# Performance work log

Measured on AMD Instinct MI355X. Metric: run time of the kernel, lower is better.

The kernel has to match this reference:

```python
import jax, jax.numpy as jnp
import numpy as np

B, T, D = 4, 1024, 512
H, TD = 4, 5
DH = D // H          # per-head value dim
DFF = D // 2         # Clifford FFN half-width
DR = D               # reservoir size
M = 64               # 2**mem_depth leaves
OFFSETS = (-3, -2, -1, 0)  # causal sheaf window=3
EPS = 1e-5

def _ln(x, g, b):
    m = jnp.mean(x, axis=-1, keepdims=True)
    v = jnp.mean((x - m) ** 2, axis=-1, keepdims=True)
    return (x - m) / jnp.sqrt(v + EPS) * g + b

def setup_inputs() -> dict:
    keys = iter(jax.random.split(jax.random.key(0), 64))
    def rn(shape, s=0.02):
        return (jax.random.normal(next(keys), shape) * s).astype(jnp.float32)
    x = jax.random.normal(next(keys), (B, T, D), dtype=jnp.float32)
    # sparse reservoir recurrence matrix (sparsity=0.9)
    wres_mask = (jax.random.uniform(next(keys), (DR, DR)) > 0.9).astype(jnp.float32)
    res_Wres = jax.random.normal(next(keys), (DR, DR)) * wres_mask * 0.05
    eye = jnp.eye(D, dtype=jnp.float32)
    sheaf_Rw = jnp.stack([eye + rn((D, D), 0.01) for _ in OFFSETS])  # [4,D,D]
    return dict(
        x=x,
        ln1_g=jnp.ones((D,)), ln1_b=jnp.zeros((D,)),
        ln2_g=jnp.ones((D,)), ln2_b=jnp.zeros((D,)),
        ln3_g=jnp.ones((D,)), ln3_b=jnp.zeros((D,)),
        ln4_g=jnp.ones((D,)), ln4_b=jnp.zeros((D,)),
        attn_Wp=rn((H * TD, D)), attn_bp=jnp.zeros((H * TD,)),
        attn_Wv=rn((D, D)), attn_Wo=rn((D, D)),
        ffn_Wr=rn((DFF, D)), ffn_br=jnp.zeros((DFF,)),
        ffn_Wi=rn((DFF, D)), ffn_bi=jnp.zeros((DFF,)),
        ffn_Wg=rn((D, D)), ffn_bg=jnp.zeros((D,)),
        ffn_Wout=rn((D, D)), ffn_bout=jnp.zeros((D,)),
        res_Win=rn((DR, D)), res_Wres=res_Wres,
        res_logrho=jnp.float32(0.0), res_leak=jnp.float32(0.3),
        res_readout=rn((D, DR)),
        res_v0=jax.random.normal(next(keys), (DR,), dtype=jnp.float32),
        mem_keys=rn((M, D)), mem_vals=rn((M, D)),
        mem_Wq=rn((D, D)), mem_Wout=rn((D, D)), mem_bout=jnp.zeros((D,)),
        sheaf_Rw=sheaf_Rw, sheaf_Rb=jnp.zeros((len(OFFSETS), D)),
        sheaf_alpha=jnp.float32(0.15),
    )

def reference(x, ln1_g, ln1_b, ln2_g, ln2_b, ln3_g, ln3_b, ln4_g, ln4_b,
              attn_Wp, attn_bp, attn_Wv, attn_Wo,
              ffn_Wr, ffn_br, ffn_Wi, ffn_bi, ffn_Wg, ffn_bg, ffn_Wout, ffn_bout,
              res_Win, res_Wres, res_logrho, res_leak, res_readout, res_v0,
              mem_keys, mem_vals, mem_Wq, mem_Wout, mem_bout,
              sheaf_Rw, sheaf_Rb, sheaf_alpha):
    Bx, Tx, d = x.shape

    def attn_fn(h):  # PAdicAttention, causal
        paths = jax.nn.sigmoid(h @ attn_Wp.T + attn_bp)
        paths = paths.reshape(Bx, Tx, H, TD).transpose(0, 2, 1, 3)   # [B,H,T,TD]
        pq = paths[:, :, :, None, :]
        pk = paths[:, :, None, :, :]
        agree = pq * pk + (1.0 - pq) * (1.0 - pk)                    # [B,H,T,T,TD]
        sim = jnp.sum(jnp.cumprod(agree, axis=-1), axis=-1) / TD     # [B,H,T,T]
        mask = jnp.triu(jnp.ones((Tx, Tx), bool), 1)
        sim = jnp.where(mask[None, None], -jnp.inf, sim)
        a = jax.nn.softmax(sim, axis=-1)
        V = (h @ attn_Wv.T).reshape(Bx, Tx, H, DH).transpose(0, 2, 1, 3)
        ctx = jnp.einsum('bhqk,bhkd->bhqd', a, V)
        return ctx.transpose(0, 2, 1, 3).reshape(Bx, Tx, d) @ attn_Wo.T

    def res_fn(h):  # EchoStateReservoir
        rho_t = jax.nn.sigmoid(res_logrho) * 1.5
        Wd = jax.lax.stop_gradient(res_Wres)
        def pi(v, _):
            v = Wd @ v
            n = jnp.linalg.norm(v)
            return jnp.where(n > 0, v / n, v), None
        v, _ = jax.lax.scan(pi, res_v0, None, length=3)
        rho_c = jax.lax.stop_gradient(jnp.linalg.norm(Wd @ v))
        Ws = res_Wres * (rho_t / jnp.maximum(rho_c, 1e-6))
        lk = jax.nn.sigmoid(res_leak)
        u = h @ res_Win.T                                            # [B,T,dr]
        def step(hs, ut):
            hs = (1.0 - lk) * hs + lk * jnp.tanh(hs @ Ws.T + ut)
            return hs, hs
        _, Hs = jax.lax.scan(step, jnp.zeros((Bx, DR), x.dtype), u.transpose(1, 0, 2))
        return Hs.transpose(1, 0, 2) @ res_readout.T

    def mem_fn(h):  # PAdicMemory
        q = h @ mem_Wq.T
        w = jax.nn.softmax(q @ mem_keys.T / jnp.sqrt(jnp.float32(d)), axis=-1)
        return (w @ mem_vals) @ mem_Wout.T + mem_bout

    def ffn_fn(h):  # CliffordFFN
        r = h @ ffn_Wr.T + ffn_br
        i = h @ ffn_Wi.T + ffn_bi
        prod = jnp.concatenate([r * r - i * i, 2.0 * r * i], axis=-1)
        gate = jax.nn.sigmoid(h @ ffn_Wg.T + ffn_bg)
        return (prod * gate) @ ffn_Wout.T + ffn_bout

    def sheaf_fn(h):  # SheafDiffusion, causal offsets
        lap = jnp.zeros_like(h)
        for idx, delta in enumerate(OFFSETS):
            Rx = h @ sheaf_Rw[idx].T + sheaf_Rb[idx]
            if delta == 0:
                x_nb = h
            else:
                ad = -delta
                x_nb = jnp.concatenate(
                    [jnp.zeros((Bx, ad, d), h.dtype), h[:, :Tx - ad, :]], axis=1)
            lap = lap + (Rx - x_nb) @ sheaf_Rw[idx]   # note: @ W, not W.T (as in source)
        return h - jnp.abs(sheaf_alpha) * lap

    x = x + attn_fn(_ln(x, ln1_g, ln1_b))
    x = x + res_fn(_ln(x, ln2_g, ln2_b))
    x = x + mem_fn(_ln(x, ln3_g, ln3_b))
    x = x + ffn_fn(_ln(x, ln4_g, ln4_b))
    return sheaf_fn(x)
```

## Files before the change

kernel.cpp:

```cpp
#include <hip/hip_runtime.h>
#include <hip/hip_bf16.h>
#include <stdint.h>

typedef unsigned short u16;
typedef unsigned int u32;
typedef unsigned long long u64;
typedef __bf16 bf16x8 __attribute__((ext_vector_type(8)));
typedef float f32x4 __attribute__((ext_vector_type(4)));
typedef int i32x4 __attribute__((ext_vector_type(4)));

__device__ __forceinline__ u16 f2bf(float f){
  unsigned u = __float_as_uint(f);
  u += 0x7fffu + ((u>>16)&1u);
  return (u16)(u>>16);
}
__device__ __forceinline__ float bf2f(u16 h){ return __uint_as_float((u32)h<<16); }
__device__ __forceinline__ float sigm(float x){ return 1.f/(1.f+__expf(-x)); }
__device__ __forceinline__ float tanh_fast(float x){ float e = __expf(2.f*x); return 1.f - 2.f/(e+1.f); }

__device__ __forceinline__ void gl_lds16(const void* g, void* l){
  __builtin_amdgcn_global_load_lds((const __attribute__((address_space(1))) void*)g,
                                   (__attribute__((address_space(3))) void*)l, 16, 0, 0);
}


__global__ __launch_bounds__(128) void prep_weights(
  const float* Wp, const float* Wv, const float* Wo, const float* Win, const float* rd,
  const float* Wq, const float* keys, const float* vals, const float* mWo,
  const float* Wr, const float* Wi, const float* Wg, const float* fWo, const float* Rw,
  const float* bp, const float* fbr, const float* fbi, const float* fbg,
  u16* WpB, u16* WvB, u16* WoB, u16* WinB, u16* rdB,
  u16* WqB, u16* keysB, u16* valsB, u16* mWoB,
  u16* WrB, u16* WiB, u16* WgB, u16* fWoB, u16* RwB,
  float* bpp, float* bpc, float* ss)
{
  int blk = blockIdx.x, t = threadIdx.x;
  if(blk==6912){ if(t<128) bpp[t] = (t<20)? bp[t] : 0.f; return; }
  if(blk==6913){
    for(int j=t; j<1024; j+=128)
      bpc[j] = (j<256)? fbr[j] : (j<512)? fbi[j-256] : fbg[j-512];
    return;
  }
  if(blk==6914){ if(t==0) ss[0]=1.f; else if(t<5) ss[t]=0.f; return; }
  const float* src = nullptr; u16* dst = nullptr; int r;
  bool perm = false;
  if(blk<128){ r=blk; dst=WpB+(size_t)r*512; if(r<20) src=Wp+(size_t)r*512; }
  else if(blk<640){ r=blk-128; dst=WvB+(size_t)r*512; src=Wv+(size_t)r*512; }
  else if(blk<1152){ r=blk-640; dst=WoB+(size_t)r*512; src=Wo+(size_t)r*512; }
  else if(blk<1664){ r=blk-1152; dst=WinB+(size_t)r*512; src=Win+(size_t)r*512; }
  else if(blk<2176){ r=blk-1664; dst=rdB+(size_t)r*512; src=rd+(size_t)r*512; perm=true; }
  else if(blk<2688){ r=blk-2176; dst=WqB+(size_t)r*512; src=Wq+(size_t)r*512; }
  else if(blk<2752){ r=blk-2688; dst=keysB+(size_t)r*512; src=keys+(size_t)r*512; }
  else if(blk<2816){ r=blk-2752; dst=valsB+(size_t)r*512; src=vals+(size_t)r*512; }
  else if(blk<3328){ r=blk-2816; dst=mWoB+(size_t)r*512; src=mWo+(size_t)r*512; }
  else if(blk<3584){ r=blk-3328; dst=WrB+(size_t)r*512; src=Wr+(size_t)r*512; }
  else if(blk<3840){ r=blk-3584; dst=WiB+(size_t)r*512; src=Wi+(size_t)r*512; }
  else if(blk<4352){ r=blk-3840; dst=WgB+(size_t)r*512; src=Wg+(size_t)r*512; }
  else if(blk<4864){ r=blk-4352; dst=fWoB+(size_t)r*512; src=fWo+(size_t)r*512; }
  else { r=blk-4864; dst=RwB+(size_t)r*512; src=Rw+(size_t)r*512; }
  if(src){
    float4 a = *(const float4*)&src[t*4];
    ushort4 o; o.x=f2bf(a.x); o.y=f2bf(a.y); o.z=f2bf(a.z); o.w=f2bf(a.w);
    if(perm){
      int k0 = t*4;
      int base = (k0 & ~63) | ((k0&15)<<2) | ((k0>>4)&3);
      dst[base] = o.x; dst[base+4] = o.y; dst[base+8] = o.z; dst[base+12] = o.w;
    } else {
      *(ushort4*)&dst[t*4] = o;
    }
  } else {
    ushort4 z; z.x=0; z.y=0; z.z=0; z.w=0;
    *(ushort4*)&dst[t*4] = z;
  }
}

__global__ __launch_bounds__(256) void transpose_rw(const float* __restrict__ Rw, u16* __restrict__ RwT){
  __shared__ float tl[32][33];
  int z = blockIdx.z, it = blockIdx.x, jt = blockIdx.y;
  const float* src = Rw + (size_t)z*262144;
  int r = threadIdx.x>>3, c4 = (threadIdx.x&7)*4;
  float4 v = *(const float4*)&src[(size_t)(jt*32+r)*512 + it*32 + c4];
  tl[r][c4+0]=v.x; tl[r][c4+1]=v.y; tl[r][c4+2]=v.z; tl[r][c4+3]=v.w;
  __syncthreads();
  ushort4 o;
  o.x = f2bf(tl[c4+0][r]); o.y = f2bf(tl[c4+1][r]);
  o.z = f2bf(tl[c4+2][r]); o.w = f2bf(tl[c4+3][r]);
  *(ushort4*)&RwT[(size_t)(it*32+r)*2048 + z*512 + jt*32 + c4] = o;
}

__global__ __launch_bounds__(64) void ln_kernel(const float* __restrict__ x, const float* __restrict__ g,
      const float* __restrict__ b, u16* __restrict__ out)
{
  int row = blockIdx.x, lane = threadIdx.x;
  const float* xr = x + (size_t)row*512;
  float4 v0 = *(const float4*)&xr[lane*4];
  float4 v1 = *(const float4*)&xr[256+lane*4];
  float s = v0.x+v0.y+v0.z+v0.w + v1.x+v1.y+v1.z+v1.w;
  float q = v0.x*v0.x+v0.y*v0.y+v0.z*v0.z+v0.w*v0.w + v1.x*v1.x+v1.y*v1.y+v1.z*v1.z+v1.w*v1.w;
  #pragma unroll
  for(int m=1;m<64;m<<=1){ s += __shfl_xor(s,m); q += __shfl_xor(q,m); }
  float mean = s*(1.f/512.f);
  float var  = q*(1.f/512.f) - mean*mean;
  float rstd = rsqrtf(var + 1e-5f);
  float4 g0 = *(const float4*)&g[lane*4], g1 = *(const float4*)&g[256+lane*4];
  float4 b0 = *(const float4*)&b[lane*4], b1 = *(const float4*)&b[256+lane*4];
  ushort4 o0, o1;
  o0.x = f2bf((v0.x-mean)*rstd*g0.x + b0.x); o0.y = f2bf((v0.y-mean)*rstd*g0.y + b0.y);
  o0.z = f2bf((v0.z-mean)*rstd*g0.z + b0.z); o0.w = f2bf((v0.w-mean)*rstd*g0.w + b0.w);
  o1.x = f2bf((v1.x-mean)*rstd*g1.x + b1.x); o1.y = f2bf((v1.y-mean)*rstd*g1.y + b1.y);
  o1.z = f2bf((v1.z-mean)*rstd*g1.z + b1.z); o1.w = f2bf((v1.w-mean)*rstd*g1.w + b1.w);
  *(ushort4*)&out[(size_t)row*512 + lane*4] = o0;
  *(ushort4*)&out[(size_t)row*512 + 256 + lane*4] = o1;
}

template<int EPI>
__global__ __launch_bounds__(256,2) void gemm_nt(
  const u16* __restrict__ A, const u16* __restrict__ Bw, int K, int ldc,
  float* __restrict__ outf, u16* __restrict__ outb,
  const float* __restrict__ bias, const float* __restrict__ resid,
  const float* __restrict__ aux, float* __restrict__ outf2,
  const float* __restrict__ scal, int shift_ad)
{
  __shared__ u16 Al[128*64];
  __shared__ u16 Bl[64*64];
  const int t = threadIdx.x;
  const int bm = blockIdx.x, bn = blockIdx.y;
  const int wid = t>>6, lane = t&63;
  const int wr = wid>>1, wc = wid&1;
  const int fr = lane&15, fq = lane>>4;
  f32x4 acc[4][2] = {};
  const int nK = K>>6;
  const u16* Ab = A + (size_t)(bm*128)*K;
  const u16* Bb = Bw + (size_t)(bn*64)*K;
  const int srow8 = t>>3;
  const int scol = (t&7)*8;
  char* AlB = (char*)Al; char* BlB = (char*)Bl;
  const int lbase = wid*1024;
  for(int bk=0; bk<nK; ++bk){
    #pragma unroll
    for(int c=0;c<4;++c)
      gl_lds16(&Ab[(size_t)(c*32+srow8)*K + bk*64 + scol], AlB + c*4096 + lbase);
    #pragma unroll
    for(int c=0;c<2;++c)
      gl_lds16(&Bb[(size_t)(c*32+srow8)*K + bk*64 + scol], BlB + c*4096 + lbase);
    __syncthreads();
    #pragma unroll
    for(int kk=0;kk<2;++kk){
      bf16x8 af[4], bf[2];
      #pragma unroll
      for(int m=0;m<4;++m) af[m] = *(const bf16x8*)&Al[(wr*64+m*16+fr)*64 + kk*32 + fq*8];
      #pragma unroll
      for(int n=0;n<2;++n) bf[n] = *(const bf16x8*)&Bl[(wc*32+n*16+fr)*64 + kk*32 + fq*8];
      #pragma unroll
      for(int m=0;m<4;++m)
        #pragma unroll
        for(int n=0;n<2;++n)
          acc[m][n] = __builtin_amdgcn_mfma_f32_16x16x32_bf16(af[m], bf[n], acc[m][n], 0,0,0);
    }
    __syncthreads();
  }
  float alpha = 0.f;
  if(EPI==8) alpha = fabsf(scal[0]);
  #pragma unroll
  for(int m=0;m<4;++m){
    int gr0 = bm*128 + wr*64 + m*16 + fq*4;
    #pragma unroll
    for(int n=0;n<2;++n){
      int gc = bn*64 + wc*32 + n*16 + fr;
      float bv = 0.f;
      if(EPI==2||EPI==3||EPI==5||EPI==6||EPI==9||EPI==12) bv = bias[gc];
      if(EPI==10 && gc<128) bv = bias[gc];
      #pragma unroll
      for(int i=0;i<4;++i){
        int r = gr0 + i;
        float v = acc[m][n][i] + bv;
        if(EPI==3) v = sigm(v);
        if(EPI==1||EPI==5||EPI==6) v += resid[(size_t)r*ldc + gc];
        if(EPI==8){
          outf[(size_t)r*ldc + gc] -= alpha*v;
        } else if(EPI==9){
          if(gc<512) outf[(size_t)r*512 + gc] = v;
          else       outf2[(size_t)r*512 + gc-512] = sigm(v);
        } else if(EPI==10){
          if(gc<128) outf[(size_t)r*128 + gc] = sigm(v);
          else       outf2[(size_t)r*512 + gc-128] = v;
        } else if(EPI==11){
          int pc = (gc & ~63) | ((gc&15)<<2) | ((gc>>4)&3);
          outf[(size_t)r*512 + pc] = v;
        } else if(EPI==12){
          int idx = gc>>9;
          int ad = 3 - idx;
          int ts = r & 1023;
          float xnb = 0.f;
          if(ts >= ad) xnb = bf2f(((const u16*)aux)[(size_t)(r-ad)*512 + (gc&511)]);
          outb[(size_t)r*2048 + gc] = f2bf(v - xnb);
        } else {
          if(EPI==0||EPI==1||EPI==2||EPI==3||EPI==5) outf[(size_t)r*ldc + gc] = v;
          if(EPI==6) outf2[(size_t)r*ldc + gc] = v;
          if(EPI==4||EPI==6) outb[(size_t)r*ldc + gc] = f2bf(v);
        }
      }
    }
  }
}

__global__ __launch_bounds__(128) void attn_kernel(
  const float* __restrict__ paths, const float* __restrict__ Vbuf, u16* __restrict__ ctxb)
{
  const int t = threadIdx.x;
  const int qt = blockIdx.x, bh = blockIdx.y;
  const int b = bh>>2, h = bh&3;
  const int rb = b<<10;
  const int ql = t>>2, sub = t&3;
  const int q = qt*32 + ql;
  const int wid = t>>6, lane = t&63;
  const int fr = lane&15, fq = lane>>4;
  __shared__ u16 Vl[128][72];
  __shared__ u16 Pl[32][72];
  __shared__ float pkl[64][6];
  __shared__ float scl[32];
  __shared__ float lsm[32];
  float al[5], bl[5];
  #pragma unroll
  for(int l=0;l<5;++l){
    float p = paths[(size_t)(rb+q)*128 + h*5 + l];
    al[l] = 2.f*p - 1.f; bl[l] = 1.f - p;
  }
  float m_run = -1e30f, l_run = 0.f;
  f32x4 acc[2][4] = {};
  const int nkt = (qt>>1) + 1;
  for(int kt=0; kt<nkt; ++kt){
    int k0 = kt*64;
    for(int i=t; i<320; i+=128){
      int k = i/5, l = i%5;
      pkl[k][l] = paths[(size_t)(rb+k0+k)*128 + h*5 + l];
    }
    {
      int dg = (t&31)*4, kbase = t>>5;
      #pragma unroll
      for(int i=0;i<16;++i){
        int k = kbase + i*4;
        float4 v4 = *(const float4*)&Vbuf[(size_t)(rb+k0+k)*512 + h*128 + dg];
        Vl[dg+0][k] = f2bf(v4.x); Vl[dg+1][k] = f2bf(v4.y);
        Vl[dg+2][k] = f2bf(v4.z); Vl[dg+3][k] = f2bf(v4.w);
      }
    }
    __syncthreads();
    float pj[16]; float tm = -1e30f;
    #pragma unroll
    for(int j=0;j<16;++j){
      int kidx = sub*16 + j;
      int k = k0 + kidx;
      float s;
      if(k <= q){
        float c = al[0]*pkl[kidx][0] + bl[0];
        float sa = c;
        #pragma unroll
        for(int l=1;l<5;++l){ c *= al[l]*pkl[kidx][l] + bl[l]; sa += c; }
        s = sa*0.2f;
      } else s = -1e30f;
      pj[j] = s; tm = fmaxf(tm, s);
    }
    tm = fmaxf(tm, __shfl_xor(tm,1,4));
    tm = fmaxf(tm, __shfl_xor(tm,2,4));
    float m_new = fmaxf(m_run, tm);
    float corr = __expf(m_run - m_new);
    float ls = 0.f;
    #pragma unroll
    for(int j=0;j<16;++j){
      float p = (pj[j] > -1e29f) ? __expf(pj[j]-m_new) : 0.f;
      ls += p;
      Pl[ql][sub*16+j] = f2bf(p);
    }
    l_run = l_run*corr + ls;
    m_run = m_new;
    if(sub==0) scl[ql] = corr;
    __syncthreads();
    #pragma unroll
    for(int m=0;m<2;++m){
      float c0 = scl[m*16+fq*4+0], c1 = scl[m*16+fq*4+1];
      float c2 = scl[m*16+fq*4+2], c3 = scl[m*16+fq*4+3];
      #pragma unroll
      for(int n=0;n<4;++n){ acc[m][n][0]*=c0; acc[m][n][1]*=c1; acc[m][n][2]*=c2; acc[m][n][3]*=c3; }
    }
    #pragma unroll
    for(int kk=0;kk<2;++kk){
      bf16x8 af[2], bf[4];
      #pragma unroll
      for(int m=0;m<2;++m) af[m] = *(const bf16x8*)&Pl[m*16+fr][kk*32+fq*8];
      #pragma unroll
      for(int n=0;n<4;++n) bf[n] = *(const bf16x8*)&Vl[wid*64+n*16+fr][kk*32+fq*8];
      #pragma unroll
      for(int m=0;m<2;++m)
        #pragma unroll
        for(int n=0;n<4;++n)
          acc[m][n] = __builtin_amdgcn_mfma_f32_16x16x32_bf16(af[m], bf[n], acc[m][n], 0,0,0);
    }
    __syncthreads();
  }
  {
    float lt = l_run + __shfl_xor(l_run,1,4);
    lt += __shfl_xor(lt,2,4);
    if(sub==0) lsm[ql] = lt;
  }
  __syncthreads();
  #pragma unroll
  for(int m=0;m<2;++m){
    float inv[4];
    #pragma unroll
    for(int i=0;i<4;++i) inv[i] = 1.f/lsm[m*16+fq*4+i];
    #pragma unroll
    for(int n=0;n<4;++n){
      int row = rb + qt*32 + m*16 + fq*4;
      int col = h*128 + wid*64 + n*16 + fr;
      #pragma unroll
      for(int i=0;i<4;++i)
        ctxb[(size_t)(row+i)*512 + col] = f2bf(acc[m][n][i]*inv[i]);
    }
  }
}

__global__ __launch_bounds__(256) void pmv(const float* __restrict__ W, const float* __restrict__ vin,
                    const float* __restrict__ ssin, float* __restrict__ vout, float* __restrict__ ssout)
{
  __shared__ float vs[512];
  int t = threadIdx.x;
  int j = blockIdx.x*16 + (t>>4), ks = t&15;
  float s = ssin[0];
  float inv = (s>0.f)? rsqrtf(s) : 1.f;
  vs[t] = vin[t]*inv; vs[t+256] = vin[t+256]*inv;
  __syncthreads();
  float p = 0.f;
  const float* wr = &W[(size_t)j*512 + ks*32];
  #pragma unroll
  for(int kk=0;kk<32;++kk) p += wr[kk]*vs[ks*32+kk];
  p += __shfl_xor(p,1,16); p += __shfl_xor(p,2,16); p += __shfl_xor(p,4,16); p += __shfl_xor(p,8,16);
  if(ks==0){ vout[j] = p; atomicAdd(ssout, p*p); }
}

__global__ __launch_bounds__(128) void scale_ws(const float* __restrict__ Wres, const float* __restrict__ ss4,
                         const float* __restrict__ logrho, signed char* __restrict__ WsQ,
                         float* __restrict__ wscale)
{
  __shared__ float wmax[2];
  int j = blockIdx.x, t = threadIdx.x;
  int fr = t&15, blk = t>>4;
  float rho_t = 1.5f * sigm(logrho[0]);
  float rho_c = sqrtf(ss4[0]);
  float sc = rho_t / fmaxf(rho_c, 1e-6f);
  float w[4];
  #pragma unroll
  for(int cg=0;cg<4;++cg) w[cg] = Wres[(size_t)j*512 + blk*64 + cg*16 + fr]*sc;
  float m = fmaxf(fmaxf(fabsf(w[0]),fabsf(w[1])), fmaxf(fabsf(w[2]),fabsf(w[3])));
  #pragma unroll
  for(int d=1; d<64; d<<=1) m = fmaxf(m, __shfl_xor(m, d));
  if((t&63)==0) wmax[t>>6] = m;
  __syncthreads();
  float rm = fmaxf(wmax[0], wmax[1]);
  float qs = (rm > 0.f) ? rm*(1.f/127.f) : 1.f;
  float inv = 1.f/qs;
  int q0 = __float2int_rn(w[0]*inv), q1 = __float2int_rn(w[1]*inv);
  int q2 = __float2int_rn(w[2]*inv), q3 = __float2int_rn(w[3]*inv);
  q0 = min(127,max(-127,q0)); q1 = min(127,max(-127,q1));
  q2 = min(127,max(-127,q2)); q3 = min(127,max(-127,q3));
  u32 pk = (u32)(q0&0xff) | ((u32)(q1&0xff)<<8) | ((u32)(q2&0xff)<<16) | ((u32)(q3&0xff)<<24);
  *(u32*)&WsQ[(size_t)j*512 + blk*64 + fr*4] = pk;
  if(t==0) wscale[j] = qs*(1.f/127.f);
}

__global__ __launch_bounds__(512) void scan_kernel(
  const signed char* __restrict__ WsQ, const float* __restrict__ wscale,
  const float* __restrict__ u, const float* __restrict__ leak_p,
  u16* __restrict__ HsB)
{
  const int t = threadIdx.x;
  const int w = t>>6, lane = t&63, fr = lane&15, fq = lane>>4;
  const int colb = w*64;
  const float lk = sigm(leak_p[0]);
  const float omlk = 1.f - lk;
  __shared__ signed char Sl[2][16*512];
  for(int i=t; i<4096; i+=512) ((u32*)Sl)[i] = 0u;
  float mysc[4];
  i32x4 bw[4][8];
  #pragma unroll
  for(int cg=0; cg<4; ++cg){
    int col = colb + cg*16 + fr;
    mysc[cg] = wscale[col];
    #pragma unroll
    for(int ks=0; ks<8; ++ks)
      bw[cg][ks] = *(const i32x4*)&WsQ[(size_t)col*512 + ks*64 + fq*16];
  }
  #pragma unroll
  for(int cg=0; cg<4; ++cg)
    #pragma unroll
    for(int ks=0; ks<8; ++ks)
      asm volatile("" : "+v"(bw[cg][ks]));
  float hp[4];
  #pragma unroll
  for(int cg=0;cg<4;++cg) hp[cg]=0.f;
  const float* up = u + (size_t)(fq*1024)*512 + colb + fr*4;
  u16* hsp = HsB + (size_t)(fq*1024)*512 + colb + fr*4;
  float4 uvc = *(const float4*)up;  up += 512;
  const int rdswz = ((fr&3)<<4) ^ (((fr>>2)&3)<<6);
  const int woff = (4*fq)*512 + ((colb + fr*4) ^ (fq<<6));
  __syncthreads();
  for(int ts=0; ts<1024; ++ts){
    float4 uvn = *(const float4*)up;  up += 512;
    const signed char* Sb = Sl[ts&1];
    i32x4 af[8];
    #pragma unroll
    for(int ks=0; ks<8; ++ks)
      af[ks] = *(const i32x4*)&Sb[fr*512 + ((ks*64 + fq*16) ^ rdswz)];
    i32x4 accA[4], accB[4];
    #pragma unroll
    for(int cg=0;cg<4;++cg){ i32x4 z = {0,0,0,0}; accA[cg] = z; accB[cg] = z; }
    #pragma unroll
    for(int ks=0;ks<4;++ks)
      #pragma unroll
      for(int cg=0;cg<4;++cg){
        accA[cg] = __builtin_amdgcn_mfma_i32_16x16x64_i8(af[ks],   bw[cg][ks],   accA[cg], 0,0,0);
        accB[cg] = __builtin_amdgcn_mfma_i32_16x16x64_i8(af[ks+4], bw[cg][ks+4], accB[cg], 0,0,0);
      }
    float h[4];
    float uu[4] = {uvc.x, uvc.y, uvc.z, uvc.w};
    #pragma unroll
    for(int cg=0;cg<4;++cg){
      float pre = (float)(accA[cg][0] + accB[cg][0])*mysc[cg] + uu[cg];
      h[cg] = omlk*hp[cg] + lk*tanh_fast(pre);
      hp[cg] = h[cg];
    }
    int q0 = __float2int_rn(h[0]*127.f), q1 = __float2int_rn(h[1]*127.f);
    int q2 = __float2int_rn(h[2]*127.f), q3 = __float2int_rn(h[3]*127.f);
    u32 qp = (u32)(q0&0xff) | ((u32)(q1&0xff)<<8) | ((u32)(q2&0xff)<<16) | ((u32)q3<<24);
    *(u32*)&Sl[(ts+1)&1][woff] = qp;
    u32 p01, p23;
    asm volatile("v_cvt_pk_bf16_f32 %0, %1, %2" : "=v"(p01) : "v"(h[0]), "v"(h[1]));
    asm volatile("v_cvt_pk_bf16_f32 %0, %1, %2" : "=v"(p23) : "v"(h[2]), "v"(h[3]));
    uint2 hv; hv.x = p01; hv.y = p23;
    *(uint2*)hsp = hv;  hsp += 512;
    uvc = uvn;
    asm volatile("s_waitcnt lgkmcnt(0)" ::: "memory");
    __builtin_amdgcn_s_barrier();
    asm volatile("" ::: "memory");
  }
}

__global__ __launch_bounds__(256) void mem_kernel(
  const u16* __restrict__ qb, const u16* __restrict__ keysB, const u16* __restrict__ valsB,
  u16* __restrict__ ctx2b)
{
  const int t = threadIdx.x, rt = blockIdx.x;
  const int wid = t>>6, lane = t&63, fr = lane&15, fq = lane>>4;
  __shared__ float S[64][65];
  __shared__ u16 Pl[64][72];
  __shared__ u16 VT[256][72];
  {
    f32x4 accs[4] = {};
    for(int ks=0; ks<16; ++ks){
      bf16x8 bfrag = *(const bf16x8*)&keysB[(size_t)(wid*16+fr)*512 + ks*32 + fq*8];
      #pragma unroll
      for(int mt=0;mt<4;++mt){
        bf16x8 afrag = *(const bf16x8*)&qb[(size_t)(rt*64+mt*16+fr)*512 + ks*32 + fq*8];
        accs[mt] = __builtin_amdgcn_mfma_f32_16x16x32_bf16(afrag, bfrag, accs[mt], 0,0,0);
      }
    }
    #pragma unroll
    for(int mt=0;mt<4;++mt)
      #pragma unroll
      for(int i=0;i<4;++i)
        S[mt*16+fq*4+i][wid*16+fr] = accs[mt][i];
  }
  __syncthreads();
  if(t<64){
    float m = -1e30f;
    for(int j=0;j<64;++j) m = fmaxf(m, S[t][j]);
    const float scale = 0.04419417382f;
    float sum = 0.f;
    for(int j=0;j<64;++j){ float p = __expf((S[t][j]-m)*scale); sum += p; S[t][j] = p; }
    float inv = 1.f/sum;
    for(int j=0;j<64;++j) Pl[t][j] = f2bf(S[t][j]*inv);
  }
  __syncthreads();
  for(int pass=0; pass<2; ++pass){
    {
      int k = t&63, cb = t>>6;
      #pragma unroll
      for(int i=0;i<8;++i){
        int d0 = (cb + i*4)*8;
        uint4 v = *(const uint4*)&valsB[(size_t)k*512 + pass*256 + d0];
        VT[d0+0][k]=(u16)(v.x); VT[d0+1][k]=(u16)(v.x>>16);
        VT[d0+2][k]=(u16)(v.y); VT[d0+3][k]=(u16)(v.y>>16);
        VT[d0+4][k]=(u16)(v.z); VT[d0+5][k]=(u16)(v.z>>16);
        VT[d0+6][k]=(u16)(v.w); VT[d0+7][k]=(u16)(v.w>>16);
      }
    }
    __syncthreads();
    f32x4 accp[4][4] = {};
    #pragma unroll
    for(int kk=0;kk<2;++kk){
      bf16x8 af[4], bf[4];
      #pragma unroll
      for(int mt=0;mt<4;++mt) af[mt] = *(const bf16x8*)&Pl[mt*16+fr][kk*32+fq*8];
      #pragma unroll
      for(int nt=0;nt<4;++nt) bf[nt] = *(const bf16x8*)&VT[wid*64+nt*16+fr][kk*32+fq*8];
      #pragma unroll
      for(int mt=0;mt<4;++mt)
        #pragma unroll
        for(int nt=0;nt<4;++nt)
          accp[mt][nt] = __builtin_amdgcn_mfma_f32_16x16x32_bf16(af[mt], bf[nt], accp[mt][nt], 0,0,0);
    }
    #pragma unroll
    for(int mt=0;mt<4;++mt)
      #pragma unroll
      for(int nt=0;nt<4;++nt){
        int row = rt*64 + mt*16 + fq*4;
        int col = pass*256 + wid*64 + nt*16 + fr;
        #pragma unroll
        for(int i=0;i<4;++i)
          ctx2b[(size_t)(row+i)*512 + col] = f2bf(accp[mt][nt][i]);
      }
    __syncthreads();
  }
}

__global__ __launch_bounds__(256) void prodgate(const float* __restrict__ ri, const float* __restrict__ g,
                         u16* __restrict__ pgb)
{
  int gi = blockIdx.x*256 + threadIdx.x;
  int row = gi>>7, c4 = (gi&127)*4;
  const float* base = ri + (size_t)row*512;
  float4 gv = *(const float4*)&g[(size_t)row*512 + c4];
  float4 o;
  if(c4 < 256){
    float4 r = *(const float4*)&base[c4];
    float4 ii = *(const float4*)&base[256+c4];
    o.x = (r.x*r.x - ii.x*ii.x)*gv.x; o.y = (r.y*r.y - ii.y*ii.y)*gv.y;
    o.z = (r.z*r.z - ii.z*ii.z)*gv.z; o.w = (r.w*r.w - ii.w*ii.w)*gv.w;
  } else {
    float4 r = *(const float4*)&base[c4-256];
    float4 ii = *(const float4*)&base[c4];
    o.x = 2.f*r.x*ii.x*gv.x; o.y = 2.f*r.y*ii.y*gv.y;
    o.z = 2.f*r.z*ii.z*gv.z; o.w = 2.f*r.w*ii.w*gv.w;
  }
  ushort4 us; us.x=f2bf(o.x); us.y=f2bf(o.y); us.z=f2bf(o.z); us.w=f2bf(o.w);
  *(ushort4*)&pgb[(size_t)row*512 + c4] = us;
}

static void launch_gemm(int epi, dim3 grid, const u16* A, const u16* B, int K, int ldc,
  float* outf, u16* outb, const float* bias, const float* resid, const float* aux,
  float* outf2, const float* scal, int ad, hipStream_t s)
{
  switch(epi){
    case 0: gemm_nt<0><<<grid,256,0,s>>>(A,B,K,ldc,outf,outb,bias,resid,aux,outf2,scal,ad); break;
    case 1: gemm_nt<1><<<grid,256,0,s>>>(A,B,K,ldc,outf,outb,bias,resid,aux,outf2,scal,ad); break;
    case 4: gemm_nt<4><<<grid,256,0,s>>>(A,B,K,ldc,outf,outb,bias,resid,aux,outf2,scal,ad); break;
    case 5: gemm_nt<5><<<grid,256,0,s>>>(A,B,K,ldc,outf,outb,bias,resid,aux,outf2,scal,ad); break;
    case 6: gemm_nt<6><<<grid,256,0,s>>>(A,B,K,ldc,outf,outb,bias,resid,aux,outf2,scal,ad); break;
    case 8: gemm_nt<8><<<grid,256,0,s>>>(A,B,K,ldc,outf,outb,bias,resid,aux,outf2,scal,ad); break;
    case 9: gemm_nt<9><<<grid,256,0,s>>>(A,B,K,ldc,outf,outb,bias,resid,aux,outf2,scal,ad); break;
    case 10: gemm_nt<10><<<grid,256,0,s>>>(A,B,K,ldc,outf,outb,bias,resid,aux,outf2,scal,ad); break;
    case 11: gemm_nt<11><<<grid,256,0,s>>>(A,B,K,ldc,outf,outb,bias,resid,aux,outf2,scal,ad); break;
    case 12: gemm_nt<12><<<grid,256,0,s>>>(A,B,K,ldc,outf,outb,bias,resid,aux,outf2,scal,ad); break;
  }
}

extern "C" void kernel_launch(void* const* d_in, const int* in_sizes, int n_in,
                              void* d_out, int out_size, void* d_ws, size_t ws_size,
                              hipStream_t stream)
{
  const float* x      = (const float*)d_in[0];
  const float* ln1g   = (const float*)d_in[1];  const float* ln1b = (const float*)d_in[2];
  const float* ln2g   = (const float*)d_in[3];  const float* ln2b = (const float*)d_in[4];
  const float* ln3g   = (const float*)d_in[5];  const float* ln3b = (const float*)d_in[6];
  const float* ln4g   = (const float*)d_in[7];  const float* ln4b = (const float*)d_in[8];
  const float* aWp    = (const float*)d_in[9];  const float* abp  = (const float*)d_in[10];
  const float* aWv    = (const float*)d_in[11]; const float* aWo  = (const float*)d_in[12];
  const float* fWr    = (const float*)d_in[13]; const float* fbr  = (const float*)d_in[14];
  const float* fWi    = (const float*)d_in[15]; const float* fbi  = (const float*)d_in[16];
  const float* fWg    = (const float*)d_in[17]; const float* fbg  = (const float*)d_in[18];
  const float* fWo    = (const float*)d_in[19]; const float* fbo  = (const float*)d_in[20];
  const float* rWin   = (const float*)d_in[21]; const float* rWres= (const float*)d_in[22];
  const float* rlogr  = (const float*)d_in[23]; const float* rleak= (const float*)d_in[24];
  const float* rread  = (const float*)d_in[25]; const float* rv0  = (const float*)d_in[26];
  const float* mkeys  = (const float*)d_in[27]; const float* mvals= (const float*)d_in[28];
  const float* mWq    = (const float*)d_in[29]; const float* mWo  = (const float*)d_in[30];
  const float* mbo    = (const float*)d_in[31];
  const float* sRw    = (const float*)d_in[32]; const float* sRb  = (const float*)d_in[33];
  const float* salpha = (const float*)d_in[34];
  (void)in_sizes; (void)n_in; (void)out_size;

  char* ws = (char*)d_ws;
  float* XCUR  = (float*)(ws + 0);
  u16*   X4B   = (u16*)  (ws + 8388608);
  u16*   HB    = (u16*)  (ws + 8388608);
  float* VU    = (float*)(ws + 12582912);
  u16*   TBUF  = (u16*)  (ws + 12582912);
  float* PATHS = (float*)(ws + 20971520);
  u16*   CTXB  = (u16*)  (ws + 23068672);
  u16*   HSB   = (u16*)  (ws + 27262976);
  char* WB = ws + 31457280;
  u16* WpB   = (u16*)(WB + 0);
  u16* WvB   = (u16*)(WB + 131072);
  u16* WoB   = (u16*)(WB + 655360);
  u16* WinB  = (u16*)(WB + 1179648);
  u16* rdB   = (u16*)(WB + 1703936);
  u16* WqB   = (u16*)(WB + 2228224);
  u16* keysB = (u16*)(WB + 2752512);
  u16* valsB = (u16*)(WB + 2818048);
  u16* mWoB  = (u16*)(WB + 2883584);
  u16* WrB   = (u16*)(WB + 3407872);
  u16* WiB   = (u16*)(WB + 3670016);
  u16* WgB   = (u16*)(WB + 3932160);
  u16* fWoB  = (u16*)(WB + 4456448);
  u16* RwB   = (u16*)(WB + 4980736);
  u16* RwTB  = (u16*)(WB + 7077888);
  signed char* WsQ = (signed char*)(WB + 9175040);
  float* wscale = (float*)(WB + 9437184);
  float* bpp = (float*)(WB + 9699328);
  float* bpc = (float*)(WB + 9699840);
  float* ssv = (float*)(WB + 9733632);
  float* vr  = (float*)(WB + 9733696);
  float* GATE = (float*)d_out;

  if(ws_size < (size_t)41200000) return;

  prep_weights<<<6915,128,0,stream>>>(aWp,aWv,aWo,rWin,rread,mWq,mkeys,mvals,mWo,fWr,fWi,fWg,fWo,sRw,
      abp, fbr, fbi, fbg,
      WpB,WvB,WoB,WinB,rdB,WqB,keysB,valsB,mWoB,WrB,WiB,WgB,fWoB,RwB,bpp,bpc,ssv);
  transpose_rw<<<dim3(16,16,4),256,0,stream>>>(sRw, RwTB);

  dim3 g512(32,8), g640(32,10), g1024(32,16), g2048(32,32);

  ln_kernel<<<4096,64,0,stream>>>(x, ln1g, ln1b, HB);
  launch_gemm(10, g640, HB, WpB, 512, 0, PATHS, nullptr, bpp, nullptr, nullptr, VU, nullptr, 0, stream);
  attn_kernel<<<dim3(32,16),128,0,stream>>>(PATHS, VU, CTXB);
  launch_gemm(1, g512, CTXB, WoB, 512, 512, XCUR, nullptr, nullptr, x, nullptr, nullptr, nullptr, 0, stream);

  ln_kernel<<<4096,64,0,stream>>>(XCUR, ln2g, ln2b, HB);
  launch_gemm(11, g512, HB, WinB, 512, 512, VU, nullptr, nullptr, nullptr, nullptr, nullptr, nullptr, 0, stream);
  pmv<<<32,256,0,stream>>>(rWres, rv0,   &ssv[0], &vr[0],    &ssv[1]);
  pmv<<<32,256,0,stream>>>(rWres, &vr[0],   &ssv[1], &vr[512],  &ssv[2]);
  pmv<<<32,256,0,stream>>>(rWres, &vr[512], &ssv[2], &vr[1024], &ssv[3]);
  pmv<<<32,256,0,stream>>>(rWres, &vr[1024],&ssv[3], &vr[1536], &ssv[4]);
  scale_ws<<<512,128,0,stream>>>(rWres, &ssv[4], rlogr, WsQ, wscale);
  scan_kernel<<<1,512,0,stream>>>(WsQ, wscale, VU, rleak, HSB);
  launch_gemm(1, g512, HSB, rdB, 512, 512, XCUR, nullptr, nullptr, XCUR, nullptr, nullptr, nullptr, 0, stream);

  ln_kernel<<<4096,64,0,stream>>>(XCUR, ln3g, ln3b, HB);
  launch_gemm(4, g512, HB, WqB, 512, 512, nullptr, CTXB, nullptr, nullptr, nullptr, nullptr, nullptr, 0, stream);
  mem_kernel<<<64,256,0,stream>>>(CTXB, keysB, valsB, HSB);
  launch_gemm(5, g512, HSB, mWoB, 512, 512, XCUR, nullptr, mbo, XCUR, nullptr, nullptr, nullptr, 0, stream);

  ln_kernel<<<4096,64,0,stream>>>(XCUR, ln4g, ln4b, HB);
  launch_gemm(9, g1024, HB, WrB, 512, 0, VU, nullptr, bpc, nullptr, nullptr, GATE, nullptr, 0, stream);
  prodgate<<<2048,256,0,stream>>>(VU, GATE, CTXB);
  launch_gemm(6, g512, CTXB, fWoB, 512, 512, nullptr, X4B, fbo, XCUR, nullptr, (float*)d_out, nullptr, 0, stream);

  launch_gemm(12, g2048, X4B, RwB, 512, 0, nullptr, TBUF, sRb, nullptr, (const float*)X4B, nullptr, nullptr, 0, stream);
  launch_gemm(8, g512, TBUF, RwTB, 2048, 512, (float*)d_out, nullptr, nullptr, nullptr, nullptr, nullptr, salpha, 0, stream);
}
```

Baseline: 1.203 ms.

## Replace per-step barrier in reservoir scan with per-wave LDS flags

The reservoir scan kernel no longer calls a workgroup barrier after each time step. Each wave now publishes a progress flag in LDS once it has written its quantized state slice. Consumer waves read the K-slices in a rotated order, starting with their own slice, and spin on the producer's flag before loading each of the others. This lets waves start MFMA work on slices that are ready instead of waiting for the slowest wave. The cost is spin-wait polling and relaxed-ordering correctness risk, including possible write-after-read hazards on the double buffer, since nothing stops a fast wave from overwriting a slice two steps ahead.

```diff
diff --git a/kernel.cpp b/kernel.cpp
--- a/kernel.cpp
+++ b/kernel.cpp
@@ -379,7 +379,9 @@
   const float lk = sigm(leak_p[0]);
   const float omlk = 1.f - lk;
   __shared__ signed char Sl[2][16*512];
+  __shared__ u32 flg[8*16];
   for(int i=t; i<4096; i+=512) ((u32*)Sl)[i] = 0u;
+  if(t < 8) flg[t*16] = 0u;
   float mysc[4];
   i32x4 bw[4][8];
   #pragma unroll
@@ -387,14 +389,16 @@
     int col = colb + cg*16 + fr;
     mysc[cg] = wscale[col];
     #pragma unroll
-    for(int ks=0; ks<8; ++ks)
-      bw[cg][ks] = *(const i32x4*)&WsQ[(size_t)col*512 + ks*64 + fq*16];
+    for(int j=0; j<8; ++j){
+      int ks = (w + j) & 7;
+      bw[cg][j] = *(const i32x4*)&WsQ[(size_t)col*512 + ks*64 + fq*16];
+    }
   }
   #pragma unroll
   for(int cg=0; cg<4; ++cg)
     #pragma unroll
-    for(int ks=0; ks<8; ++ks)
-      asm volatile("" : "+v"(bw[cg][ks]));
+    for(int j=0; j<8; ++j)
+      asm volatile("" : "+v"(bw[cg][j]));
   float hp[4];
   #pragma unroll
   for(int cg=0;cg<4;++cg) hp[cg]=0.f;
@@ -407,20 +411,30 @@
   for(int ts=0; ts<1024; ++ts){
     float4 uvn = *(const float4*)up;  up += 512;
     const signed char* Sb = Sl[ts&1];
-    i32x4 af[8];
-    #pragma unroll
-    for(int ks=0; ks<8; ++ks)
-      af[ks] = *(const i32x4*)&Sb[fr*512 + ((ks*64 + fq*16) ^ rdswz)];
     i32x4 accA[4], accB[4];
     #pragma unroll
     for(int cg=0;cg<4;++cg){ i32x4 z = {0,0,0,0}; accA[cg] = z; accB[cg] = z; }
     #pragma unroll
-    for(int ks=0;ks<4;++ks)
-      #pragma unroll
-      for(int cg=0;cg<4;++cg){
-        accA[cg] = __builtin_amdgcn_mfma_i32_16x16x64_i8(af[ks],   bw[cg][ks],   accA[cg], 0,0,0);
-        accB[cg] = __builtin_amdgcn_mfma_i32_16x16x64_i8(af[ks+4], bw[cg][ks+4], accB[cg], 0,0,0);
+    for(int j=0;j<8;++j){
+      int ks = (w + j) & 7;
+      if(j > 0){
+        u32 f;
+        do {
+          f = __hip_atomic_load(&flg[ks*16], __ATOMIC_RELAXED, __HIP_MEMORY_SCOPE_WORKGROUP);
+        } while(f < (u32)ts);
       }
+      __builtin_amdgcn_sched_barrier(0);
+      i32x4 af = *(const i32x4*)&Sb[fr*512 + ((ks*64 + fq*16) ^ rdswz)];
+      if(j & 1){
+        #pragma unroll
+        for(int cg=0;cg<4;++cg)
+          accB[cg] = __builtin_amdgcn_mfma_i32_16x16x64_i8(af, bw[cg][j], accB[cg], 0,0,0);
+      } else {
+        #pragma unroll
+        for(int cg=0;cg<4;++cg)
+          accA[cg] = __builtin_amdgcn_mfma_i32_16x16x64_i8(af, bw[cg][j], accA[cg], 0,0,0);
+      }
+    }
     float h[4];
     float uu[4] = {uvc.x, uvc.y, uvc.z, uvc.w};
     #pragma unroll
@@ -433,15 +447,15 @@
     int q2 = __float2int_rn(h[2]*127.f), q3 = __float2int_rn(h[3]*127.f);
     u32 qp = (u32)(q0&0xff) | ((u32)(q1&0xff)<<8) | ((u32)(q2&0xff)<<16) | ((u32)q3<<24);
     *(u32*)&Sl[(ts+1)&1][woff] = qp;
+    asm volatile("s_waitcnt lgkmcnt(0)" ::: "memory");
+    if(lane == 0)
+      __hip_atomic_store(&flg[w*16], (u32)(ts+1), __ATOMIC_RELAXED, __HIP_MEMORY_SCOPE_WORKGROUP);
     u32 p01, p23;
     asm volatile("v_cvt_pk_bf16_f32 %0, %1, %2" : "=v"(p01) : "v"(h[0]), "v"(h[1]));
     asm volatile("v_cvt_pk_bf16_f32 %0, %1, %2" : "=v"(p23) : "v"(h[2]), "v"(h[3]));
     uint2 hv; hv.x = p01; hv.y = p23;
     *(uint2*)hsp = hv;  hsp += 512;
     uvc = uvn;
-    asm volatile("s_waitcnt lgkmcnt(0)" ::: "memory");
-    __builtin_amdgcn_s_barrier();
-    asm volatile("" ::: "memory");
   }
 }
 
```

Measured after the change: 1.669 ms. 1.39x slower.

## Split reservoir scan across 16 waves with 2 columns per lane

Applied to the files above, without the earlier changes.

The single-block sequential reservoir scan now runs with 1024 threads (16 waves) instead of 512. Each lane owns 2 output columns instead of 4, with a remapped column permutation, so per-step MFMA chains and register-resident weight tiles are halved per wave. The intent is to shorten the serial per-timestep critical path of this latency-bound recurrence. The cost is a barrier across twice as many waves each step and more LDS read traffic, since every wave reloads the full A fragment.

```diff
diff --git a/kernel.cpp b/kernel.cpp
--- a/kernel.cpp
+++ b/kernel.cpp
@@ -368,76 +368,79 @@
   if(t==0) wscale[j] = qs*(1.f/127.f);
 }
 
-__global__ __launch_bounds__(512) void scan_kernel(
+__global__ __launch_bounds__(1024) void scan_kernel(
   const signed char* __restrict__ WsQ, const float* __restrict__ wscale,
   const float* __restrict__ u, const float* __restrict__ leak_p,
   u16* __restrict__ HsB)
 {
   const int t = threadIdx.x;
   const int w = t>>6, lane = t&63, fr = lane&15, fq = lane>>4;
-  const int colb = w*64;
   const float lk = sigm(leak_p[0]);
   const float omlk = 1.f - lk;
   __shared__ signed char Sl[2][16*512];
-  for(int i=t; i<4096; i+=512) ((u32*)Sl)[i] = 0u;
-  float mysc[4];
-  i32x4 bw[4][8];
-  #pragma unroll
-  for(int cg=0; cg<4; ++cg){
-    int col = colb + cg*16 + fr;
-    mysc[cg] = wscale[col];
+  for(int i=t; i<4096; i+=1024) ((u32*)Sl)[i] = 0u;
+  const int pbase = w*32 + fr*2;
+  float mysc[2];
+  i32x4 bw[2][8];
+  #pragma unroll
+  for(int cg=0; cg<2; ++cg){
+    int pc = pbase + cg;
+    int oc = (pc & ~63) | ((pc&3)<<4) | ((pc>>2)&15);
+    mysc[cg] = wscale[oc];
     #pragma unroll
     for(int ks=0; ks<8; ++ks)
-      bw[cg][ks] = *(const i32x4*)&WsQ[(size_t)col*512 + ks*64 + fq*16];
-  }
-  #pragma unroll
-  for(int cg=0; cg<4; ++cg)
+      bw[cg][ks] = *(const i32x4*)&WsQ[(size_t)oc*512 + ks*64 + fq*16];
+  }
+  #pragma unroll
+  for(int cg=0; cg<2; ++cg)
     #pragma unroll
     for(int ks=0; ks<8; ++ks)
       asm volatile("" : "+v"(bw[cg][ks]));
-  float hp[4];
-  #pragma unroll
-  for(int cg=0;cg<4;++cg) hp[cg]=0.f;
-  const float* up = u + (size_t)(fq*1024)*512 + colb + fr*4;
-  u16* hsp = HsB + (size_t)(fq*1024)*512 + colb + fr*4;
-  float4 uvc = *(const float4*)up;  up += 512;
+  float hp0 = 0.f, hp1 = 0.f;
+  const float* up = u + (size_t)(fq*1024)*512 + pbase;
+  u16* hsp = HsB + (size_t)(fq*1024)*512 + pbase;
+  float2 uvc = *(const float2*)up;  up += 512;
   const int rdswz = ((fr&3)<<4) ^ (((fr>>2)&3)<<6);
-  const int woff = (4*fq)*512 + ((colb + fr*4) ^ (fq<<6));
+  const int woff = (4*fq)*512 + (pbase ^ (fq<<6));
   __syncthreads();
   for(int ts=0; ts<1024; ++ts){
-    float4 uvn = *(const float4*)up;  up += 512;
+    float2 uvn = *(const float2*)up;  up += 512;
     const signed char* Sb = Sl[ts&1];
-    i32x4 af[8];
-    #pragma unroll
-    for(int ks=0; ks<8; ++ks)
-      af[ks] = *(const i32x4*)&Sb[fr*512 + ((ks*64 + fq*16) ^ rdswz)];
-    i32x4 accA[4], accB[4];
-    #pragma unroll
-    for(int cg=0;cg<4;++cg){ i32x4 z = {0,0,0,0}; accA[cg] = z; accB[cg] = z; }
-    #pragma unroll
-    for(int ks=0;ks<4;++ks)
-      #pragma unroll
-      for(int cg=0;cg<4;++cg){
-        accA[cg] = __builtin_amdgcn_mfma_i32_16x16x64_i8(af[ks],   bw[cg][ks],   accA[cg], 0,0,0);
-        accB[cg] = __builtin_amdgcn_mfma_i32_16x16x64_i8(af[ks+4], bw[cg][ks+4], accB[cg], 0,0,0);
+    i32x4 accA[2], accB[2];
+    { i32x4 z = {0,0,0,0}; accA[0]=z; accA[1]=z; accB[0]=z; accB[1]=z; }
+    {
+      i32x4 af[4];
+      #pragma unroll
+      for(int ks=0; ks<4; ++ks)
+        af[ks] = *(const i32x4*)&Sb[fr*512 + ((ks*64 + fq*16) ^ rdswz)];
+      #pragma unroll
+      for(int ks=0; ks<4; ++ks){
+        accA[0] = __builtin_amdgcn_mfma_i32_16x16x64_i8(af[ks], bw[0][ks], accA[0], 0,0,0);
+        accA[1] = __builtin_amdgcn_mfma_i32_16x16x64_i8(af[ks], bw[1][ks], accA[1], 0,0,0);
       }
-    float h[4];
-    float uu[4] = {uvc.x, uvc.y, uvc.z, uvc.w};
-    #pragma unroll
-    for(int cg=0;cg<4;++cg){
-      float pre = (float)(accA[cg][0] + accB[cg][0])*mysc[cg] + uu[cg];
-      h[cg] = omlk*hp[cg] + lk*tanh_fast(pre);
-      hp[cg] = h[cg];
-    }
-    int q0 = __float2int_rn(h[0]*127.f), q1 = __float2int_rn(h[1]*127.f);
-    int q2 = __float2int_rn(h[2]*127.f), q3 = __float2int_rn(h[3]*127.f);
-    u32 qp = (u32)(q0&0xff) | ((u32)(q1&0xff)<<8) | ((u32)(q2&0xff)<<16) | ((u32)q3<<24);
-    *(u32*)&Sl[(ts+1)&1][woff] = qp;
-    u32 p01, p23;
-    asm volatile("v_cvt_pk_bf16_f32 %0, %1, %2" : "=v"(p01) : "v"(h[0]), "v"(h[1]));
-    asm volatile("v_cvt_pk_bf16_f32 %0, %1, %2" : "=v"(p23) : "v"(h[2]), "v"(h[3]));
-    uint2 hv; hv.x = p01; hv.y = p23;
-    *(uint2*)hsp = hv;  hsp += 512;
+    }
+    {
+      i32x4 af[4];
+      #pragma unroll
+      for(int ks=0; ks<4; ++ks)
+        af[ks] = *(const i32x4*)&Sb[fr*512 + (((ks+4)*64 + fq*16) ^ rdswz)];
+      #pragma unroll
+      for(int ks=0; ks<4; ++ks){
+        accB[0] = __builtin_amdgcn_mfma_i32_16x16x64_i8(af[ks], bw[0][ks+4], accB[0], 0,0,0);
+        accB[1] = __builtin_amdgcn_mfma_i32_16x16x64_i8(af[ks], bw[1][ks+4], accB[1], 0,0,0);
+      }
+    }
+    float pre0 = (float)(accA[0][0] + accB[0][0])*mysc[0] + uvc.x;
+    float pre1 = (float)(accA[1][0] + accB[1][0])*mysc[1] + uvc.y;
+    float h0 = omlk*hp0 + lk*tanh_fast(pre0);
+    float h1 = omlk*hp1 + lk*tanh_fast(pre1);
+    hp0 = h0; hp1 = h1;
+    int q0 = __float2int_rn(h0*127.f), q1 = __float2int_rn(h1*127.f);
+    u16 qp = (u16)((q0&0xff) | ((q1&0xff)<<8));
+    *(u16*)&Sl[(ts+1)&1][woff] = qp;
+    u32 p01;
+    asm volatile("v_cvt_pk_bf16_f32 %0, %1, %2" : "=v"(p01) : "v"(h0), "v"(h1));
+    *(u32*)hsp = p01;  hsp += 512;
     uvc = uvn;
     asm volatile("s_waitcnt lgkmcnt(0)" ::: "memory");
     __builtin_amdgcn_s_barrier();
@@ -643,7 +646,7 @@
   pmv<<<32,256,0,stream>>>(rWres, &vr[512], &ssv[2], &vr[1024], &ssv[3]);
   pmv<<<32,256,0,stream>>>(rWres, &vr[1024],&ssv[3], &vr[1536], &ssv[4]);
   scale_ws<<<512,128,0,stream>>>(rWres, &ssv[4], rlogr, WsQ, wscale);
-  scan_kernel<<<1,512,0,stream>>>(WsQ, wscale, VU, rleak, HSB);
+  scan_kernel<<<1,1024,0,stream>>>(WsQ, wscale, VU, rleak, HSB);
   launch_gemm(1, g512, HSB, rdB, 512, 512, XCUR, nullptr, nullptr, XCUR, nullptr, nullptr, nullptr, 0, stream);
 
   ln_kernel<<<4096,64,0,stream>>>(XCUR, ln3g, ln3b, HB);
```

Result: faster. 1.167 ms (-3.0%).
